# Optimization experiments

Hardware: AMD Instinct MI355X
Metric: run time of the kernel (lower is better)

Reference implementation:

```python
import jax, jax.numpy as jnp
import numpy as np

N_NODES = 100000
N_EDGES = 1600000
N_GRAPHS = 1024
F_NODE = 16
F_EDGE = 8
F_GRAPH = 10
F_OUT = 1
H = 64
EPS = 1e-7  # GENConv eps
T = 1.0     # GENConv softmax temperature (learn_t=False default)


def _lin_init(key, fi, fo):
    kw, kb = jax.random.split(key)
    s = 1.0 / np.sqrt(fi)
    W = jax.random.uniform(kw, (fi, fo), jnp.float32, -s, s)
    b = jax.random.uniform(kb, (fo,), jnp.float32, -s, s)
    return W, b


def setup_inputs() -> dict:
    key = jax.random.key(0)
    ks = jax.random.split(key, 24)
    inp = {
        'x': jax.random.normal(ks[0], (N_NODES, F_NODE), jnp.float32),
        'edge_attr': jax.random.normal(ks[1], (N_EDGES, F_EDGE), jnp.float32),
        'graph_attr': jax.random.normal(ks[2], (N_GRAPHS, F_GRAPH), jnp.float32),
        'edge_index': jax.random.randint(ks[3], (2, N_EDGES), 0, N_NODES),
        'batch': jnp.sort(jax.random.randint(ks[4], (N_NODES,), 0, N_GRAPHS)),
    }
    inp['node_W'], inp['node_b'] = _lin_init(ks[5], F_NODE, H)
    inp['edge_W'], inp['edge_b'] = _lin_init(ks[6], F_EDGE, H)
    # three GENConv MLPs: Linear(H,2H) -> BN(identity @eval) -> ReLU -> Linear(2H,H)
    for i, k1, k2 in ((1, ks[7], ks[8]), (2, ks[9], ks[10]), (3, ks[11], ks[12])):
        inp[f'c{i}_W1'], inp[f'c{i}_b1'] = _lin_init(k1, H, 2 * H)
        inp[f'c{i}_W2'], inp[f'c{i}_b2'] = _lin_init(k2, 2 * H, H)
    inp['d1_W'], inp['d1_b'] = _lin_init(ks[13], H + F_GRAPH, 32)
    inp['d2_W'], inp['d2_b'] = _lin_init(ks[14], 32, 32)
    inp['out_W'], inp['out_b'] = _lin_init(ks[15], 32, F_OUT)
    return inp


def _genconv(h, src, dst, ea, W1, b1, W2, b2):
    # message: relu(x_j + edge_attr) + eps   [E, H]
    msg = jax.nn.relu(h[src] + ea) + EPS
    # per-destination, per-feature segment softmax (aggr='softmax', t=1)
    m = jax.ops.segment_max(msg * T, dst, num_segments=N_NODES)   # [N, H]
    e = jnp.exp(msg * T - m[dst])                                  # [E, H]
    denom = jax.ops.segment_sum(e, dst, num_segments=N_NODES)     # [N, H]
    alpha = e / jnp.maximum(denom[dst], 1e-16)
    agg = jax.ops.segment_sum(msg * alpha, dst, num_segments=N_NODES)
    out = h + agg  # root add
    # MLP (BatchNorm is identity in eval with default stats)
    hid = jax.nn.relu(out @ W1 + b1)
    return hid @ W2 + b2


def reference(x, edge_attr, graph_attr, node_W, node_b, edge_W, edge_b,
              c1_W1, c1_b1, c1_W2, c1_b2,
              c2_W1, c2_b1, c2_W2, c2_b2,
              c3_W1, c3_b1, c3_W2, c3_b2,
              d1_W, d1_b, d2_W, d2_b, out_W, out_b,
              edge_index, batch):
    src, dst = edge_index[0], edge_index[1]
    h = x @ node_W + node_b
    ea = edge_attr @ edge_W + edge_b
    h = jax.nn.relu(_genconv(h, src, dst, ea, c1_W1, c1_b1, c1_W2, c1_b2))
    h = jax.nn.relu(_genconv(h, src, dst, ea, c2_W1, c2_b1, c2_W2, c2_b2))
    h = jax.nn.relu(_genconv(h, src, dst, ea, c3_W1, c3_b1, c3_W2, c3_b2))
    # global mean pool over graphs
    sums = jax.ops.segment_sum(h, batch, num_segments=N_GRAPHS)          # [G, H]
    cnt = jax.ops.segment_sum(jnp.ones((h.shape[0],), h.dtype), batch, num_segments=N_GRAPHS)
    pooled = sums / jnp.maximum(cnt, 1.0)[:, None]
    g = jnp.concatenate([pooled, graph_attr], axis=1)                    # [G, H+F_GRAPH]
    g = jax.nn.relu(g @ d1_W + d1_b)   # dropout = identity at eval
    g = jax.nn.relu(g @ d2_W + d2_b)
    return jax.nn.sigmoid(g @ out_W + out_b)                             # [G, 1]
```

## Files before the change

kernel.cpp:

```cpp
#include <hip/hip_runtime.h>
#include <hip/hip_bf16.h>

#define N_NODES 100000
#define N_EDGES 1600000
#define N_GRAPHS 1024
#define F_NODE 16
#define F_EDGE 8
#define F_GRAPH 10
#define HD 64
#define HD2 128
#define GEN_EPS 1e-7f
#define SCAN_NBLK ((N_NODES + 255) / 256)

typedef unsigned short u16;
typedef unsigned int u32;
typedef __attribute__((ext_vector_type(8))) short short8;
typedef __attribute__((ext_vector_type(4))) float floatx4;

__device__ __forceinline__ u16 f2bf(float x) {
    u32 u = __float_as_uint(x);
    return (u16)((u + 0x7FFFu + ((u >> 16) & 1u)) >> 16);
}
__device__ __forceinline__ float bf2f(u16 u) {
    return __uint_as_float(((u32)u) << 16);
}
__device__ __forceinline__ float u2f(unsigned int u) {
    return __uint_as_float(u);
}

__global__ void __launch_bounds__(256) k_node_embed(
        const float* __restrict__ x, const float* __restrict__ W,
        const float* __restrict__ b, float* __restrict__ h,
        u16* __restrict__ hb) {
    __shared__ float sW[F_NODE * HD];
    __shared__ float sb[HD];
    for (int i = threadIdx.x; i < F_NODE * HD; i += 256) sW[i] = W[i];
    if (threadIdx.x < HD) sb[threadIdx.x] = b[threadIdx.x];
    __syncthreads();
    int t = blockIdx.x * 256 + threadIdx.x;
    if (t >= N_NODES * HD) return;
    int n = t >> 6, f = t & 63;
    const float* xr = x + (size_t)n * F_NODE;
    float acc = sb[f];
#pragma unroll
    for (int k = 0; k < F_NODE; k++) acc += xr[k] * sW[k * HD + f];
    h[t] = acc;
    hb[t] = f2bf(acc);
}

__global__ void __launch_bounds__(256) k_hist(
        const int* __restrict__ dst, int* __restrict__ deg,
        int* __restrict__ rank) {
    int e = blockIdx.x * 256 + threadIdx.x;
    if (e >= N_EDGES) return;
    rank[e] = atomicAdd(&deg[dst[e]], 1);
}

__global__ void __launch_bounds__(256) k_scan1(
        const int* __restrict__ deg, int* __restrict__ bsum) {
    __shared__ int red[256];
    int t = threadIdx.x;
    int g = blockIdx.x * 256 + t;
    red[t] = (g < N_NODES) ? deg[g] : 0;
    __syncthreads();
    for (int s = 128; s > 0; s >>= 1) {
        if (t < s) red[t] += red[t + s];
        __syncthreads();
    }
    if (t == 0) bsum[blockIdx.x] = red[0];
}

__global__ void __launch_bounds__(512) k_scan2(
        const int* __restrict__ bsum, int* __restrict__ bpre) {
    __shared__ int sh[512];
    int t = threadIdx.x;
    int v = (t < SCAN_NBLK) ? bsum[t] : 0;
    sh[t] = v;
    __syncthreads();
    for (int d = 1; d < 512; d <<= 1) {
        int u = (t >= d) ? sh[t - d] : 0;
        __syncthreads();
        sh[t] += u;
        __syncthreads();
    }
    if (t < SCAN_NBLK) bpre[t] = sh[t] - v;
}

__global__ void __launch_bounds__(256) k_scan3(
        const int* __restrict__ deg, const int* __restrict__ bpre,
        int* __restrict__ off) {
    __shared__ int sh[256];
    int t = threadIdx.x;
    int g = blockIdx.x * 256 + t;
    int v = (g < N_NODES) ? deg[g] : 0;
    sh[t] = v;
    __syncthreads();
    for (int d = 1; d < 256; d <<= 1) {
        int u = (t >= d) ? sh[t - d] : 0;
        __syncthreads();
        sh[t] += u;
        __syncthreads();
    }
    int incl = sh[t];
    int base = bpre[blockIdx.x];
    if (g < N_NODES) off[g] = base + incl - v;
    if (g == N_NODES - 1) off[N_NODES] = base + incl;
}

__global__ void __launch_bounds__(256) k_scatter(
        const int* __restrict__ src, const int* __restrict__ dst,
        const int* __restrict__ rank, const int* __restrict__ off,
        const float* __restrict__ eattr,
        unsigned int* __restrict__ rec, int* __restrict__ srcs) {
    int e = blockIdx.x * 256 + threadIdx.x;
    if (e >= N_EDGES) return;
    const uint4* ap = reinterpret_cast<const uint4*>(eattr + (size_t)e * F_EDGE);
    uint4 a0 = ap[0], a1 = ap[1];
    int pos = off[dst[e]] + rank[e];
    uint4* op = reinterpret_cast<uint4*>(rec + (size_t)pos * 8);
    op[0] = a0;
    op[1] = a1;
    srcs[pos] = src[e];
}

__global__ void __launch_bounds__(256) k_prep(
        const float* __restrict__ W1a, const float* __restrict__ W2a,
        const float* __restrict__ W1b, const float* __restrict__ W2b,
        const float* __restrict__ W1c, const float* __restrict__ W2c,
        u16* __restrict__ W1t, u16* __restrict__ W2t) {
    int bid = blockIdx.x;
    int l = bid >> 6;
    int t = (bid & 63) * 256 + threadIdx.x;
    const float* W1 = (l == 0) ? W1a : (l == 1) ? W1b : W1c;
    const float* W2 = (l == 0) ? W2a : (l == 1) ? W2b : W2c;
    if (t < HD * HD2) {
        int j = t >> 6, k = t & 63;
        W1t[(size_t)l * HD * HD2 + t] = f2bf(W1[k * HD2 + j]);
    } else {
        int u = t - HD * HD2;
        int c = u >> 7, j = u & 127;
        W2t[(size_t)l * HD * HD2 + u] = f2bf(W2[j * HD + c]);
    }
}

__global__ void __launch_bounds__(256) k_gen_agg(
        const float* __restrict__ h, const u16* __restrict__ hb,
        const int* __restrict__ off,
        const unsigned int* __restrict__ rec,
        const int* __restrict__ srcs,
        const float* __restrict__ eW, const float* __restrict__ eb,
        float* __restrict__ outb) {
    __shared__ float sAttr[4][128];
    int wid = threadIdx.x >> 6;
    int lane = threadIdx.x & 63;
    int f = lane;
    float w[F_EDGE];
#pragma unroll
    for (int k = 0; k < F_EDGE; k++) w[k] = eW[k * HD + f];
    float bfv = eb[f];
    int wave0 = blockIdx.x * 4 + wid;
    const int NW = gridDim.x * 4;
    for (int n0 = wave0; n0 < N_NODES; n0 += NW) {
        int n = __builtin_amdgcn_readfirstlane(n0);
        int beg = off[n], end = off[n + 1];
        size_t idx = (size_t)n * HD + f;
        float hroot = h[idx];
        float den = 0.f, nm = 0.f;
        if (beg < end) {
            int i = beg;
            float av0 = 0.f, av1 = 0.f;
            if (beg + (lane >> 3) < end) av0 = u2f(rec[(size_t)beg * 8 + lane]);
            if (beg + 8 + (lane >> 3) < end)
                av1 = u2f(rec[(size_t)(beg + 8) * 8 + lane]);
            int s16[16];
#pragma unroll
            for (int u = 0; u < 16; u++) s16[u] = srcs[beg + u];
            while (true) {
                float hv[16];
#pragma unroll
                for (int u = 0; u < 16; u++)
                    hv[u] = bf2f(hb[(size_t)s16[u] * HD + f]);
                int inx = i + 16;
                bool more = inx < end;
                float av0N = 0.f, av1N = 0.f;
                int s16N[16];
                if (more) {
                    if (inx + (lane >> 3) < end)
                        av0N = u2f(rec[(size_t)inx * 8 + lane]);
                    if (inx + 8 + (lane >> 3) < end)
                        av1N = u2f(rec[(size_t)(inx + 8) * 8 + lane]);
#pragma unroll
                    for (int u = 0; u < 16; u++) s16N[u] = srcs[inx + u];
                } else {
#pragma unroll
                    for (int u = 0; u < 16; u++) s16N[u] = 0;
                }
                sAttr[wid][lane] = av0;
                sAttr[wid][64 + lane] = av1;
#pragma unroll
                for (int u = 0; u < 16; u++) {
                    if (i + u < end) {
                        const floatx4* A = reinterpret_cast<const floatx4*>(
                            &sAttr[wid][u * 8]);
                        floatx4 a0 = A[0], a1 = A[1];
                        float ea = bfv + a0.x * w[0] + a0.y * w[1]
                                       + a0.z * w[2] + a0.w * w[3]
                                       + a1.x * w[4] + a1.y * w[5]
                                       + a1.z * w[6] + a1.w * w[7];
                        float r = fmaxf(hv[u] + ea, 0.f);
                        float ev = __expf(r);
                        den += ev;
                        nm += r * ev;
                    }
                }
                if (!more) break;
                i = inx;
                av0 = av0N;
                av1 = av1N;
#pragma unroll
                for (int u = 0; u < 16; u++) s16[u] = s16N[u];
            }
        }
        float agg = (end > beg) ? (nm / fmaxf(den, 1e-16f) + GEN_EPS) : 0.f;
        outb[idx] = hroot + agg;
    }
}

__global__ void __launch_bounds__(256) k_mlp(
        const float* __restrict__ inb,
        const u16* __restrict__ W1t, const float* __restrict__ b1,
        const u16* __restrict__ W2t, const float* __restrict__ b2,
        float* __restrict__ hout, u16* __restrict__ hbout) {
    __shared__ u16 sHid[64][HD2 + 8];
    int tid = threadIdx.x;
    int wid = tid >> 6, lane = tid & 63;
    int quad = lane >> 4, lm = lane & 15;
    int n0 = blockIdx.x * 64 + wid * 16;
    if (n0 >= N_NODES) return;
    int node = n0 + lm;
    short8 a[2];
    const float* ar = inb + (size_t)node * HD;
#pragma unroll
    for (int kk = 0; kk < 2; kk++) {
        const float4* p = reinterpret_cast<const float4*>(ar + kk * 32 + quad * 8);
        float4 v0 = p[0], v1 = p[1];
        short8 t;
        t[0] = (short)f2bf(v0.x); t[1] = (short)f2bf(v0.y);
        t[2] = (short)f2bf(v0.z); t[3] = (short)f2bf(v0.w);
        t[4] = (short)f2bf(v1.x); t[5] = (short)f2bf(v1.y);
        t[6] = (short)f2bf(v1.z); t[7] = (short)f2bf(v1.w);
        a[kk] = t;
    }
#pragma unroll
    for (int jt = 0; jt < 8; jt++) {
        int jb = jt * 16;
        float bias = b1[jb + lm];
        floatx4 acc = {bias, bias, bias, bias};
#pragma unroll
        for (int kk = 0; kk < 2; kk++) {
            const short8* bp = reinterpret_cast<const short8*>(
                W1t + (size_t)(jb + lm) * HD + kk * 32 + quad * 8);
            acc = __builtin_amdgcn_mfma_f32_16x16x32_bf16(a[kk], *bp, acc, 0, 0, 0);
        }
#pragma unroll
        for (int r = 0; r < 4; r++) {
            int lr = wid * 16 + quad * 4 + r;
            sHid[lr][jb + lm] = f2bf(fmaxf(acc[r], 0.f));
        }
    }
    short8 a2[4];
#pragma unroll
    for (int kk = 0; kk < 4; kk++)
        a2[kk] = *reinterpret_cast<const short8*>(
            &sHid[wid * 16 + lm][kk * 32 + quad * 8]);
#pragma unroll
    for (int ct = 0; ct < 4; ct++) {
        int cb = ct * 16;
        float bias = b2[cb + lm];
        floatx4 acc = {bias, bias, bias, bias};
#pragma unroll
        for (int kk = 0; kk < 4; kk++) {
            const short8* bp = reinterpret_cast<const short8*>(
                W2t + (size_t)(cb + lm) * HD2 + kk * 32 + quad * 8);
            acc = __builtin_amdgcn_mfma_f32_16x16x32_bf16(a2[kk], *bp, acc, 0, 0, 0);
        }
#pragma unroll
        for (int r = 0; r < 4; r++) {
            int orow = n0 + quad * 4 + r;
            float o = fmaxf(acc[r], 0.f);
            hout[(size_t)orow * HD + cb + lm] = o;
            hbout[(size_t)orow * HD + cb + lm] = f2bf(o);
        }
    }
}

__global__ void __launch_bounds__(256) k_pool(
        const float* __restrict__ h, const int* __restrict__ batch,
        float* __restrict__ pooled) {
    int g = blockIdx.x * 4 + (threadIdx.x >> 6);
    if (g >= N_GRAPHS) return;
    int f = threadIdx.x & 63;
    int lo = 0, hi = N_NODES;
    while (lo < hi) {
        int mid = (lo + hi) >> 1;
        if (batch[mid] < g) lo = mid + 1; else hi = mid;
    }
    int b = lo;
    int lo2 = b, hi2 = N_NODES;
    while (lo2 < hi2) {
        int mid = (lo2 + hi2) >> 1;
        if (batch[mid] < g + 1) lo2 = mid + 1; else hi2 = mid;
    }
    int e = lo2;
    float s = 0.f;
    for (int n = b; n < e; n++) s += h[(size_t)n * HD + f];
    float cnt = fmaxf((float)(e - b), 1.f);
    pooled[(size_t)g * HD + f] = s / cnt;
}

__global__ void __launch_bounds__(64) k_head(
        const float* __restrict__ pooled, const float* __restrict__ gattr,
        const float* __restrict__ d1W, const float* __restrict__ d1b,
        const float* __restrict__ d2W, const float* __restrict__ d2b,
        const float* __restrict__ oW, const float* __restrict__ ob,
        float* __restrict__ out) {
    int g = blockIdx.x;
    __shared__ float si[HD + F_GRAPH];
    __shared__ float s1[32], s2[32];
    int t = threadIdx.x;
    if (t < HD) si[t] = pooled[(size_t)g * HD + t];
    if (t < F_GRAPH) si[HD + t] = gattr[(size_t)g * F_GRAPH + t];
    __syncthreads();
    if (t < 32) {
        float acc = d1b[t];
        for (int i = 0; i < HD + F_GRAPH; i++) acc += si[i] * d1W[i * 32 + t];
        s1[t] = fmaxf(acc, 0.f);
    }
    __syncthreads();
    if (t < 32) {
        float acc = d2b[t];
        for (int i = 0; i < 32; i++) acc += s1[i] * d2W[i * 32 + t];
        s2[t] = fmaxf(acc, 0.f);
    }
    __syncthreads();
    if (t == 0) {
        float acc = ob[0];
        for (int i = 0; i < 32; i++) acc += s2[i] * oW[i];
        out[g] = 1.f / (1.f + __expf(-acc));
    }
}

extern "C" void kernel_launch(void* const* d_in, const int* in_sizes, int n_in,
                              void* d_out, int out_size, void* d_ws, size_t ws_size,
                              hipStream_t stream) {
    const float* x     = (const float*)d_in[0];
    const float* eattr = (const float*)d_in[1];
    const float* gattr = (const float*)d_in[2];
    const int*   eidx  = (const int*)d_in[3];
    const int*   batch = (const int*)d_in[4];
    const float* nodeW = (const float*)d_in[5];
    const float* nodeb = (const float*)d_in[6];
    const float* edgeW = (const float*)d_in[7];
    const float* edgeb = (const float*)d_in[8];
    const float* cW1[3] = {(const float*)d_in[9],  (const float*)d_in[13], (const float*)d_in[17]};
    const float* cb1[3] = {(const float*)d_in[10], (const float*)d_in[14], (const float*)d_in[18]};
    const float* cW2[3] = {(const float*)d_in[11], (const float*)d_in[15], (const float*)d_in[19]};
    const float* cb2[3] = {(const float*)d_in[12], (const float*)d_in[16], (const float*)d_in[20]};
    const float* d1W = (const float*)d_in[21];
    const float* d1b = (const float*)d_in[22];
    const float* d2W = (const float*)d_in[23];
    const float* d2b = (const float*)d_in[24];
    const float* oW  = (const float*)d_in[25];
    const float* ob  = (const float*)d_in[26];

    const int* src = eidx;
    const int* dst = eidx + N_EDGES;

    char* p = (char*)d_ws;
    float* h      = (float*)p; p += (size_t)N_NODES * HD * 4;
    float* outb   = (float*)p; p += (size_t)N_NODES * HD * 4;
    int*   srcs   = (int*)p;   p += (size_t)(N_EDGES + 64) * 4;
    unsigned int* rec = (unsigned int*)p; p += (size_t)(N_EDGES + 8) * F_EDGE * 4;
    u16*   hb     = (u16*)p;   p += (size_t)N_NODES * HD * 2;
    u16*   W1t    = (u16*)p;   p += (size_t)3 * HD * HD2 * 2;
    u16*   W2t    = (u16*)p;   p += (size_t)3 * HD * HD2 * 2;
    float* pooled = (float*)p; p += (size_t)N_GRAPHS * HD * 4;
    int*   off    = (int*)p;   p += (size_t)(N_NODES + 1) * 4;
    int*   deg    = (int*)p;   p += (size_t)N_NODES * 4;
    int*   rank   = (int*)p;   p += (size_t)N_EDGES * 4;
    int*   bsum   = (int*)p;   p += (size_t)(SCAN_NBLK + 1) * 4;
    int*   bpre   = (int*)p;   p += (size_t)(SCAN_NBLK + 1) * 4;

    const int EB = (N_EDGES + 255) / 256;
    const int NBM = (N_NODES + 63) / 64;

    k_node_embed<<<(N_NODES * HD + 255) / 256, 256, 0, stream>>>(x, nodeW, nodeb, h, hb);
    k_prep<<<192, 256, 0, stream>>>(cW1[0], cW2[0], cW1[1], cW2[1], cW1[2], cW2[2],
                                    W1t, W2t);

    hipMemsetAsync(deg, 0, (size_t)N_NODES * 4, stream);
    hipMemsetAsync(srcs + N_EDGES, 0, 64 * sizeof(int), stream);
    k_hist<<<EB, 256, 0, stream>>>(dst, deg, rank);
    k_scan1<<<SCAN_NBLK, 256, 0, stream>>>(deg, bsum);
    k_scan2<<<1, 512, 0, stream>>>(bsum, bpre);
    k_scan3<<<SCAN_NBLK, 256, 0, stream>>>(deg, bpre, off);
    k_scatter<<<EB, 256, 0, stream>>>(src, dst, rank, off, eattr, rec, srcs);

    for (int l = 0; l < 3; l++) {
        k_gen_agg<<<2048, 256, 0, stream>>>(
            h, hb, off, rec, srcs, edgeW, edgeb, outb);
        k_mlp<<<NBM, 256, 0, stream>>>(outb,
                                       W1t + (size_t)l * HD * HD2, cb1[l],
                                       W2t + (size_t)l * HD * HD2, cb2[l],
                                       h, hb);
    }

    k_pool<<<(N_GRAPHS + 3) / 4, 256, 0, stream>>>(h, batch, pooled);
    k_head<<<N_GRAPHS, 64, 0, stream>>>(pooled, gattr,
                                        d1W, d1b, d2W, d2b, oW, ob,
                                        (float*)d_out);
}
```

Before: 712.6 us.

## Fuse histogram, node embed and weight prep into one kernel; shrink agg batch

Three independent setup kernels (degree histogram, node embedding, MLP weight transpose/convert) are merged into a single launch that dispatches on block index, cutting launch overhead and letting the three kinds of work overlap. Separately, the GENConv aggregation loop now processes 8 edges per iteration instead of 16. This lowers register pressure and wasted lanes for low-degree nodes, but halves the number of gathers kept in flight per iteration.

```diff
diff --git a/kernel.cpp b/kernel.cpp
--- a/kernel.cpp
+++ b/kernel.cpp
@@ -11,6 +11,8 @@
 #define HD2 128
 #define GEN_EPS 1e-7f
 #define SCAN_NBLK ((N_NODES + 255) / 256)
+#define EB_BLK ((N_EDGES + 255) / 256)
+#define EMB_BLK ((N_NODES * HD + 255) / 256)
 
 typedef unsigned short u16;
 typedef unsigned int u32;
@@ -28,16 +30,44 @@
     return __uint_as_float(u);
 }
 
-__global__ void __launch_bounds__(256) k_node_embed(
+__global__ void __launch_bounds__(256) k_front(
+        const int* __restrict__ dst, int* __restrict__ deg,
+        int* __restrict__ rank,
         const float* __restrict__ x, const float* __restrict__ W,
         const float* __restrict__ b, float* __restrict__ h,
-        u16* __restrict__ hb) {
+        u16* __restrict__ hb,
+        const float* __restrict__ W1a, const float* __restrict__ W2a,
+        const float* __restrict__ W1b, const float* __restrict__ W2b,
+        const float* __restrict__ W1c, const float* __restrict__ W2c,
+        u16* __restrict__ W1t, u16* __restrict__ W2t) {
+    int bid = blockIdx.x;
+    if (bid < EB_BLK) {
+        int e = bid * 256 + threadIdx.x;
+        if (e < N_EDGES) rank[e] = atomicAdd(&deg[dst[e]], 1);
+        return;
+    }
+    if (bid >= EB_BLK + EMB_BLK) {
+        int pb = bid - (EB_BLK + EMB_BLK);
+        int l = pb >> 6;
+        int t = (pb & 63) * 256 + threadIdx.x;
+        const float* W1 = (l == 0) ? W1a : (l == 1) ? W1b : W1c;
+        const float* W2 = (l == 0) ? W2a : (l == 1) ? W2b : W2c;
+        if (t < HD * HD2) {
+            int j = t >> 6, k = t & 63;
+            W1t[(size_t)l * HD * HD2 + t] = f2bf(W1[k * HD2 + j]);
+        } else {
+            int u = t - HD * HD2;
+            int c = u >> 7, j = u & 127;
+            W2t[(size_t)l * HD * HD2 + u] = f2bf(W2[j * HD + c]);
+        }
+        return;
+    }
     __shared__ float sW[F_NODE * HD];
     __shared__ float sb[HD];
     for (int i = threadIdx.x; i < F_NODE * HD; i += 256) sW[i] = W[i];
     if (threadIdx.x < HD) sb[threadIdx.x] = b[threadIdx.x];
     __syncthreads();
-    int t = blockIdx.x * 256 + threadIdx.x;
+    int t = (bid - EB_BLK) * 256 + threadIdx.x;
     if (t >= N_NODES * HD) return;
     int n = t >> 6, f = t & 63;
     const float* xr = x + (size_t)n * F_NODE;
@@ -46,14 +76,6 @@
     for (int k = 0; k < F_NODE; k++) acc += xr[k] * sW[k * HD + f];
     h[t] = acc;
     hb[t] = f2bf(acc);
-}
-
-__global__ void __launch_bounds__(256) k_hist(
-        const int* __restrict__ dst, int* __restrict__ deg,
-        int* __restrict__ rank) {
-    int e = blockIdx.x * 256 + threadIdx.x;
-    if (e >= N_EDGES) return;
-    rank[e] = atomicAdd(&deg[dst[e]], 1);
 }
 
 __global__ void __launch_bounds__(256) k_scan1(
@@ -123,26 +145,6 @@
     srcs[pos] = src[e];
 }
 
-__global__ void __launch_bounds__(256) k_prep(
-        const float* __restrict__ W1a, const float* __restrict__ W2a,
-        const float* __restrict__ W1b, const float* __restrict__ W2b,
-        const float* __restrict__ W1c, const float* __restrict__ W2c,
-        u16* __restrict__ W1t, u16* __restrict__ W2t) {
-    int bid = blockIdx.x;
-    int l = bid >> 6;
-    int t = (bid & 63) * 256 + threadIdx.x;
-    const float* W1 = (l == 0) ? W1a : (l == 1) ? W1b : W1c;
-    const float* W2 = (l == 0) ? W2a : (l == 1) ? W2b : W2c;
-    if (t < HD * HD2) {
-        int j = t >> 6, k = t & 63;
-        W1t[(size_t)l * HD * HD2 + t] = f2bf(W1[k * HD2 + j]);
-    } else {
-        int u = t - HD * HD2;
-        int c = u >> 7, j = u & 127;
-        W2t[(size_t)l * HD * HD2 + u] = f2bf(W2[j * HD + c]);
-    }
-}
-
 __global__ void __launch_bounds__(256) k_gen_agg(
         const float* __restrict__ h, const u16* __restrict__ hb,
         const int* __restrict__ off,
@@ -150,7 +152,7 @@
         const int* __restrict__ srcs,
         const float* __restrict__ eW, const float* __restrict__ eb,
         float* __restrict__ outb) {
-    __shared__ float sAttr[4][128];
+    __shared__ float sAttr[4][64];
     int wid = threadIdx.x >> 6;
     int lane = threadIdx.x & 63;
     int f = lane;
@@ -168,37 +170,32 @@
         float den = 0.f, nm = 0.f;
         if (beg < end) {
             int i = beg;
-            float av0 = 0.f, av1 = 0.f;
-            if (beg + (lane >> 3) < end) av0 = u2f(rec[(size_t)beg * 8 + lane]);
-            if (beg + 8 + (lane >> 3) < end)
-                av1 = u2f(rec[(size_t)(beg + 8) * 8 + lane]);
-            int s16[16];
-#pragma unroll
-            for (int u = 0; u < 16; u++) s16[u] = srcs[beg + u];
+            float av = 0.f;
+            if (beg + (lane >> 3) < end) av = u2f(rec[(size_t)beg * 8 + lane]);
+            int s8[8];
+#pragma unroll
+            for (int u = 0; u < 8; u++) s8[u] = srcs[beg + u];
             while (true) {
-                float hv[16];
-#pragma unroll
-                for (int u = 0; u < 16; u++)
-                    hv[u] = bf2f(hb[(size_t)s16[u] * HD + f]);
-                int inx = i + 16;
+                float hv[8];
+#pragma unroll
+                for (int u = 0; u < 8; u++)
+                    hv[u] = bf2f(hb[(size_t)s8[u] * HD + f]);
+                int inx = i + 8;
                 bool more = inx < end;
-                float av0N = 0.f, av1N = 0.f;
-                int s16N[16];
+                float avN = 0.f;
+                int s8N[8];
                 if (more) {
                     if (inx + (lane >> 3) < end)
-                        av0N = u2f(rec[(size_t)inx * 8 + lane]);
-                    if (inx + 8 + (lane >> 3) < end)
-                        av1N = u2f(rec[(size_t)(inx + 8) * 8 + lane]);
-#pragma unroll
-                    for (int u = 0; u < 16; u++) s16N[u] = srcs[inx + u];
+                        avN = u2f(rec[(size_t)inx * 8 + lane]);
+#pragma unroll
+                    for (int u = 0; u < 8; u++) s8N[u] = srcs[inx + u];
                 } else {
 #pragma unroll
-                    for (int u = 0; u < 16; u++) s16N[u] = 0;
+                    for (int u = 0; u < 8; u++) s8N[u] = 0;
                 }
-                sAttr[wid][lane] = av0;
-                sAttr[wid][64 + lane] = av1;
-#pragma unroll
-                for (int u = 0; u < 16; u++) {
+                sAttr[wid][lane] = av;
+#pragma unroll
+                for (int u = 0; u < 8; u++) {
                     if (i + u < end) {
                         const floatx4* A = reinterpret_cast<const floatx4*>(
                             &sAttr[wid][u * 8]);
@@ -215,10 +212,9 @@
                 }
                 if (!more) break;
                 i = inx;
-                av0 = av0N;
-                av1 = av1N;
-#pragma unroll
-                for (int u = 0; u < 16; u++) s16[u] = s16N[u];
+                av = avN;
+#pragma unroll
+                for (int u = 0; u < 8; u++) s8[u] = s8N[u];
             }
         }
         float agg = (end > beg) ? (nm / fmaxf(den, 1e-16f) + GEN_EPS) : 0.f;
@@ -391,20 +387,17 @@
     int*   bsum   = (int*)p;   p += (size_t)(SCAN_NBLK + 1) * 4;
     int*   bpre   = (int*)p;   p += (size_t)(SCAN_NBLK + 1) * 4;
 
-    const int EB = (N_EDGES + 255) / 256;
     const int NBM = (N_NODES + 63) / 64;
-
-    k_node_embed<<<(N_NODES * HD + 255) / 256, 256, 0, stream>>>(x, nodeW, nodeb, h, hb);
-    k_prep<<<192, 256, 0, stream>>>(cW1[0], cW2[0], cW1[1], cW2[1], cW1[2], cW2[2],
-                                    W1t, W2t);
 
     hipMemsetAsync(deg, 0, (size_t)N_NODES * 4, stream);
     hipMemsetAsync(srcs + N_EDGES, 0, 64 * sizeof(int), stream);
-    k_hist<<<EB, 256, 0, stream>>>(dst, deg, rank);
+    k_front<<<EB_BLK + EMB_BLK + 192, 256, 0, stream>>>(
+        dst, deg, rank, x, nodeW, nodeb, h, hb,
+        cW1[0], cW2[0], cW1[1], cW2[1], cW1[2], cW2[2], W1t, W2t);
     k_scan1<<<SCAN_NBLK, 256, 0, stream>>>(deg, bsum);
     k_scan2<<<1, 512, 0, stream>>>(bsum, bpre);
     k_scan3<<<SCAN_NBLK, 256, 0, stream>>>(deg, bpre, off);
-    k_scatter<<<EB, 256, 0, stream>>>(src, dst, rank, off, eattr, rec, srcs);
+    k_scatter<<<EB_BLK, 256, 0, stream>>>(src, dst, rank, off, eattr, rec, srcs);
 
     for (int l = 0; l < 3; l++) {
         k_gen_agg<<<2048, 256, 0, stream>>>(
```

New measurement: 715.9 us. No clear change (+0.5%).
